# Kernel tuning notes

Measured on AMD Instinct MI355X. Metric: run time of the kernel, lower is better.

Reference implementation:

```python
import jax, jax.numpy as jnp
import numpy as np
import math

B, T, DIN, ENC_LEN, ENC, DEC = 16384, 13, 4, 48, 60, 30

def setup_inputs() -> dict:
    key = jax.random.key(0)
    ks = jax.random.split(key, 20)
    def n(k, shape, s=0.2):
        return jax.random.normal(k, shape, dtype=jnp.float32) * s
    z = lambda *s: jnp.zeros(s, dtype=jnp.float32)
    return {
        "batch_ids": jax.random.randint(ks[0], (B,), 0, 1000),
        "y": n(ks[1], (B, T, DIN), 1.0),
        "encoder_outputs": n(ks[2], (ENC_LEN, B, ENC), 1.0),
        "hidden": n(ks[3], (B, DEC), 1.0),
        "Wq": n(ks[4], (DEC, DEC)), "bq": z(DEC),
        "Wk": n(ks[5], (DEC, ENC)), "bk": z(DEC),
        "Wv": n(ks[6], (DEC, ENC)), "bv": z(DEC),
        "Wsa1": n(ks[7], (DEC // 4, 1)), "bsa1": z(DEC // 4),
        "Wsa2": n(ks[8], (DEC, DEC // 4)), "bsa2": z(DEC),
        "Wg": n(ks[9], (DEC, 2 * DEC)), "bg": z(DEC),
        "Wf1": n(ks[10], (DEC, DEC + 1)), "bf1": z(DEC),
        "Wf2": n(ks[11], (DEC // 2, DEC)), "bf2": z(DEC // 2),
        "Wf3": n(ks[12], (1, DEC // 2)), "bf3": z(1),
        "W_ih": n(ks[13], (4 * DEC, DIN + DEC)), "b_ih": z(4 * DEC),
        "W_hh": n(ks[14], (4 * DEC, DEC)), "b_hh": z(4 * DEC),
    }

def reference(batch_ids, y, encoder_outputs, hidden, Wq, bq, Wk, bk, Wv, bv,
              Wsa1, bsa1, Wsa2, bsa2, Wg, bg, Wf1, bf1, Wf2, bf2, Wf3, bf3,
              W_ih, b_ih, W_hh, b_hh):
    y_ = jnp.transpose(y, (1, 0, 2))                       # [T,B,DIN]
    enc = jnp.transpose(encoder_outputs, (1, 0, 2))        # [B,L,ENC]
    enc_spatial = enc.mean(axis=1)                          # [B,ENC] (num_turbines=1 after unsqueeze)
    # K,V are step-independent -> hoist out of the recurrence (same math as original)
    K = enc_spatial @ Wk.T + bk                             # [B,DEC]
    V = enc_spatial @ Wv.T + bv                             # [B,DEC]
    scale = 1.0 / math.sqrt(DEC)
    rnn_in0 = jnp.nan_to_num(y_[0])                         # [B,DIN], replicates NaN->0
    cell0 = jnp.zeros_like(hidden)

    def step(carry, i):
        h, c, rin = carry                                   # [B,DEC],[B,DEC],[B,DIN]
        sr = (i.astype(jnp.float32) / 12.0).reshape(1, 1)   # step ratio
        sf = jax.nn.relu(sr @ Wsa1.T + bsa1) @ Wsa2.T + bsa2  # [1,DEC] step feature
        Q = (h + sf) @ Wq.T + bq                            # [B,DEC]
        scores = jnp.sum(K * Q, axis=-1, keepdims=True) * scale  # [B,1]
        attn = jax.nn.softmax(scores, axis=-1)              # trivially ones (single turbine)
        context = attn * V                                  # [B,DEC]
        gate = jax.nn.sigmoid(jnp.concatenate([h, context], 1) @ Wg.T + bg)
        enh = gate * h + (1.0 - gate) * context
        x = jnp.concatenate([rin, enh], 1)                  # [B,DIN+DEC]
        g = x @ W_ih.T + b_ih + h @ W_hh.T + b_hh           # [B,4*DEC]
        ig, fg, gg, og = jnp.split(g, 4, axis=1)            # torch LSTM gate order i,f,g,o
        c_new = jax.nn.sigmoid(fg) * c + jax.nn.sigmoid(ig) * jnp.tanh(gg)
        h_new = jax.nn.sigmoid(og) * jnp.tanh(c_new)
        se = jnp.broadcast_to(sr, (h_new.shape[0], 1))      # [B,1] step encoding
        zfc = jax.nn.relu(jnp.concatenate([h_new, se], 1) @ Wf1.T + bf1)
        zfc = jax.nn.relu(zfc @ Wf2.T + bf2)
        out = zfc @ Wf3.T + bf3                             # [B,1]
        nxt = jax.lax.dynamic_index_in_dim(y_, i % T, axis=0, keepdims=False)  # [B,DIN]
        rin_next = jnp.concatenate([nxt[:, 1:], out], 1)    # [B,DIN]
        return (h_new, c_new, rin_next), out

    _, outs = jax.lax.scan(step, (hidden, cell0, rnn_in0), jnp.arange(1, 13))
    return outs[:, :, 0]                                    # [12,B] = cat(dim=1).transpose(0,1)
```

## Files before the change

kernel.cpp:

```cpp
#include <hip/hip_runtime.h>
#include <math.h>

#define NB 16384
typedef _Float16 f16;
typedef _Float16 f16x8 __attribute__((ext_vector_type(8)));
typedef _Float16 f16x4 __attribute__((ext_vector_type(4)));
typedef float f32x4 __attribute__((ext_vector_type(4)));

__device__ __forceinline__ float fast_sig(float v)  { return __builtin_amdgcn_rcpf(1.0f + __expf(-v)); }
__device__ __forceinline__ float fast_tanh(float v) { return 1.0f - 2.0f * __builtin_amdgcn_rcpf(1.0f + __expf(2.0f * v)); }

#define MFMA16(A, B, C) __builtin_amdgcn_mfma_f32_16x16x32_f16(A, B, C, 0, 0, 0)
#define WBAR() __builtin_amdgcn_wave_barrier()

__global__ __launch_bounds__(256) void es_kernel(
    const float* __restrict__ enc, float* __restrict__ es)
{
    const int u = blockIdx.x * 256 + threadIdx.x;
    const float4* e4 = (const float4*)enc;
    float ax = 0.f, ay = 0.f, az = 0.f, aw = 0.f;
    #pragma unroll 8
    for (int L = 0; L < 48; ++L) {
        const float4 v = e4[(size_t)L * (NB * 15) + u];
        ax += v.x; ay += v.y; az += v.z; aw += v.w;
    }
    const float s = 1.f / 48.f;
    float4 r; r.x = ax * s; r.y = ay * s; r.z = az * s; r.w = aw * s;
    ((float4*)es)[u] = r;
}

__global__ __launch_bounds__(128, 2) void decoder_kernel(
    const float* __restrict__ y,
    const float* __restrict__ enc,
    const float* __restrict__ esrc,
    const float* __restrict__ hidden,
    const float* __restrict__ Wv,  const float* __restrict__ bv,
    const float* __restrict__ Wg,  const float* __restrict__ bg,
    const float* __restrict__ Wf1, const float* __restrict__ bf1,
    const float* __restrict__ Wf2, const float* __restrict__ bf2,
    const float* __restrict__ Wf3, const float* __restrict__ bf3,
    const float* __restrict__ Wih, const float* __restrict__ bih,
    const float* __restrict__ Whh, const float* __restrict__ bhh,
    float* __restrict__ out)
{
    __shared__ __align__(16) f16 x16[16][72];
    __shared__ __align__(16) f16 z1b[16][32];

    const int t = threadIdx.x;
    const int wid = t >> 6, l = t & 63;
    const int r = l & 15, g = l >> 4;
    const int bw = blockIdx.x * 16;
    const f32x4 kz = {0.f, 0.f, 0.f, 0.f};

    #pragma unroll
    for (int d = 0; d < 5; ++d) { const int u = d * 128 + t; if (u < 576) ((unsigned*)x16)[u] = 0u; }
    #pragma unroll
    for (int d = 0; d < 2; ++d) ((unsigned*)z1b)[d * 128 + t] = 0u;

    if (esrc) {
        const float4* s4 = (const float4*)esrc + (size_t)bw * 15;
        #pragma unroll
        for (int s = 0; s < 2; ++s) {
            const int u = s * 128 + t;
            if (u < 240) {
                const float4 v = s4[u];
                const int row = u / 15, q4 = u - row * 15;
                f16x4 h = {(f16)v.x, (f16)v.y, (f16)v.z, (f16)v.w};
                *(f16x4*)&x16[row][q4 * 4] = h;
            }
        }
    } else {
        const float4* e4 = (const float4*)enc + (size_t)bw * 15;
        const float sc = 1.f / 48.f;
        #pragma unroll 1
        for (int s = 0; s < 2; ++s) {
            const int u = s * 128 + t;
            if (u < 240) {
                const int row = u / 15, q4 = u - row * 15;
                float ax = 0.f, ay = 0.f, az = 0.f, aw = 0.f;
                for (int L = 0; L < 48; ++L) {
                    const float4 v = e4[(size_t)L * (NB * 15) + u];
                    ax += v.x; ay += v.y; az += v.z; aw += v.w;
                }
                f16x4 h = {(f16)(ax*sc), (f16)(ay*sc), (f16)(az*sc), (f16)(aw*sc)};
                *(f16x4*)&x16[row][q4 * 4] = h;
            }
        }
    }

    f16x8 lf[2][8], gf[2][2], vf[2][2], f1f[2], f2f, f3f;
    float bl[8], bgv[2], bv0 = 0.f, bv1 = 0.f, bf1v[2], wf1se[2], bf2v = 0.f, bf3v = 0.f;
    float hD[2][4], VD[2][4], c[2][4] = {};
    float r0v[4] = {0.f, 0.f, 0.f, 0.f};

    if (wid == 0) {
        #pragma unroll
        for (int kt = 0; kt < 2; ++kt)
            #pragma unroll
            for (int tq = 0; tq < 8; ++tq) {
                const int gate = tq >> 1, j = (tq & 1) * 16 + r;
                const int trow = gate * 30 + j;
                f16x8 w;
                #pragma unroll
                for (int e = 0; e < 8; ++e) {
                    const int k = kt * 32 + g * 8 + e;
                    float val = 0.f;
                    if (j < 30) val = (k < 34) ? Wih[trow * 34 + k] : Whh[trow * 30 + (k - 34)];
                    w[e] = (f16)val;
                }
                lf[kt][tq] = w;
            }
        #pragma unroll
        for (int nt = 0; nt < 2; ++nt) {
            const int j = nt * 16 + r;
            f16x8 w0, w1;
            #pragma unroll
            for (int e = 0; e < 8; ++e) {
                const int kl = g * 8 + e;
                w0[e] = (f16)((j < 30 && kl >= 2) ? Wg[j * 60 + (kl - 2)] : 0.f);
                w1[e] = (f16)((j < 30 && kl < 30) ? Wg[j * 60 + 30 + kl] : 0.f);
            }
            gf[0][nt] = w0; gf[1][nt] = w1;
        }
        #pragma unroll
        for (int kt = 0; kt < 2; ++kt)
            #pragma unroll
            for (int nt = 0; nt < 2; ++nt) {
                const int j = nt * 16 + r;
                f16x8 w;
                #pragma unroll
                for (int e = 0; e < 8; ++e) {
                    const int kl = kt * 32 + g * 8 + e;
                    w[e] = (f16)((j < 30 && kl < 60) ? Wv[j * 60 + kl] : 0.f);
                }
                vf[kt][nt] = w;
            }
        #pragma unroll
        for (int tq = 0; tq < 8; ++tq) {
            const int gate = tq >> 1, j = (tq & 1) * 16 + r;
            bl[tq] = (j < 30) ? bih[gate * 30 + j] + bhh[gate * 30 + j] : 0.f;
        }
        #pragma unroll
        for (int nt = 0; nt < 2; ++nt) {
            const int j = nt * 16 + r;
            bgv[nt] = (j < 30) ? bg[j] : 0.f;
        }
        bv0 = bv[r];
        bv1 = (16 + r < 30) ? bv[16 + r] : 0.f;
        #pragma unroll
        for (int nt = 0; nt < 2; ++nt)
            #pragma unroll
            for (int q = 0; q < 4; ++q) {
                const int row = 4 * g + q, j = nt * 16 + r;
                hD[nt][q] = (j < 30) ? hidden[(size_t)(bw + row) * 30 + j] : 0.f;
            }
    } else {
        #pragma unroll
        for (int nt = 0; nt < 2; ++nt) {
            const int j = nt * 16 + r;
            f16x8 w;
            #pragma unroll
            for (int e = 0; e < 8; ++e) {
                const int kl = g * 8 + e;
                w[e] = (f16)((j < 30 && kl >= 2) ? Wf1[j * 31 + (kl - 2)] : 0.f);
            }
            f1f[nt] = w;
            bf1v[nt]  = (j < 30) ? bf1[j] : 0.f;
            wf1se[nt] = (j < 30) ? Wf1[j * 31 + 30] : 0.f;
        }
        #pragma unroll
        for (int e = 0; e < 8; ++e) {
            const int kl = g * 8 + e;
            f2f[e] = (f16)((r < 15 && kl < 30) ? Wf2[r * 30 + kl] : 0.f);
            f3f[e] = (f16)((r == 0 && kl < 15) ? Wf3[kl] : 0.f);
        }
        bf2v = (r < 15) ? bf2[r] : 0.f;
        bf3v = bf3[0];
        if (l < 16) {
            const float* yp = y + (size_t)(bw + l) * 52;
            #pragma unroll
            for (int d = 0; d < 4; ++d) {
                float v = yp[d];
                r0v[d] = (v == v) ? v : 0.f;
            }
        }
    }
    __syncthreads();

    f16x8 va;
    if (wid == 0) {
        const f16x8 ea0 = *(const f16x8*)((const char*)x16 + (size_t)r * 144 + g * 16);
        const f16x8 ea1 = *(const f16x8*)((const char*)x16 + (size_t)r * 144 + 64 + g * 16);
        f32x4 vd0 = MFMA16(ea0, vf[0][0], kz); vd0 = MFMA16(ea1, vf[1][0], vd0);
        f32x4 vd1 = MFMA16(ea0, vf[0][1], kz); vd1 = MFMA16(ea1, vf[1][1], vd1);
        #pragma unroll
        for (int q = 0; q < 4; ++q) { VD[0][q] = vd0[q] + bv0; VD[1][q] = vd1[q] + bv1; }
        #pragma unroll
        for (int nt = 0; nt < 2; ++nt)
            #pragma unroll
            for (int q = 0; q < 4; ++q)
                z1b[4 * g + q][nt * 16 + r] = (f16)VD[nt][q];
        WBAR();
        va = *(const f16x8*)((const char*)z1b + (size_t)r * 64 + g * 16);
    }
    __syncthreads();

    if (wid == 0) {
        #pragma unroll
        for (int nt = 0; nt < 2; ++nt)
            #pragma unroll
            for (int q = 0; q < 4; ++q)
                x16[4 * g + q][34 + nt * 16 + r] = (f16)hD[nt][q];
    } else {
        if (l < 16) {
            #pragma unroll
            for (int d = 0; d < 4; ++d)
                x16[l][d] = (f16)r0v[d];
        }
    }

    float py1 = 0.f, py2 = 0.f, py3 = 0.f;
    #pragma unroll 1
    for (int i = 1; i <= 12; ++i) {
        if (wid == 0) {
            const f16x8 xhg = *(const f16x8*)((const char*)x16 + (size_t)r * 144 + 64 + g * 16);
            f32x4 gd0 = MFMA16(xhg, gf[0][0], kz); gd0 = MFMA16(va, gf[1][0], gd0);
            f32x4 gd1 = MFMA16(xhg, gf[0][1], kz); gd1 = MFMA16(va, gf[1][1], gd1);
            #pragma unroll
            for (int nt = 0; nt < 2; ++nt)
                #pragma unroll
                for (int q = 0; q < 4; ++q) {
                    const float a  = (nt ? gd1[q] : gd0[q]) + bgv[nt];
                    const float gt = fast_sig(a);
                    const float enh = gt * hD[nt][q] + (1.f - gt) * VD[nt][q];
                    const int j = nt * 16 + r;
                    if (j < 30) x16[4 * g + q][4 + j] = (f16)enh;
                }
        } else if (i > 1) {
            const int s = i - 1;
            const float se = (float)s * (1.f / 12.f);
            {
                const f16x8 hn = *(const f16x8*)((const char*)x16 + (size_t)r * 144 + 64 + g * 16);
                f32x4 d0 = MFMA16(hn, f1f[0], kz);
                f32x4 d1 = MFMA16(hn, f1f[1], kz);
                #pragma unroll
                for (int nt = 0; nt < 2; ++nt)
                    #pragma unroll
                    for (int q = 0; q < 4; ++q) {
                        const float z = fmaxf((nt ? d1[q] : d0[q]) + bf1v[nt] + se * wf1se[nt], 0.f);
                        z1b[4 * g + q][nt * 16 + r] = (f16)z;
                    }
            }
            WBAR();
            {
                const f16x8 z1a = *(const f16x8*)((const char*)z1b + (size_t)r * 64 + g * 16);
                f32x4 d = MFMA16(z1a, f2f, kz);
                #pragma unroll
                for (int q = 0; q < 4; ++q)
                    z1b[4 * g + q][r] = (f16)fmaxf(d[q] + bf2v, 0.f);
            }
            WBAR();
            {
                const f16x8 z2a = *(const f16x8*)((const char*)z1b + (size_t)r * 64 + g * 16);
                f32x4 od = MFMA16(z2a, f3f, kz);
                if (r == 0) {
                    #pragma unroll
                    for (int q = 0; q < 4; ++q) {
                        const float o = od[q] + bf3v;
                        out[(size_t)(s - 1) * NB + bw + 4 * g + q] = o;
                        x16[4 * g + q][3] = (f16)o;
                    }
                }
            }
            if (l < 16) {
                x16[l][0] = (f16)py1;
                x16[l][1] = (f16)py2;
                x16[l][2] = (f16)py3;
            }
        }
        __syncthreads();

        if (wid == 0) {
            const f16x8 xa0 = *(const f16x8*)((const char*)x16 + (size_t)r * 144 + g * 16);
            const f16x8 xa1 = *(const f16x8*)((const char*)x16 + (size_t)r * 144 + 64 + g * 16);
            f32x4 ld[8];
            #pragma unroll
            for (int tq = 0; tq < 8; ++tq) {
                ld[tq] = MFMA16(xa0, lf[0][tq], kz);
                ld[tq] = MFMA16(xa1, lf[1][tq], ld[tq]);
            }
            #pragma unroll
            for (int jh = 0; jh < 2; ++jh)
                #pragma unroll
                for (int q = 0; q < 4; ++q) {
                    const float ii = fast_sig (ld[0 + jh][q] + bl[0 + jh]);
                    const float ff = fast_sig (ld[2 + jh][q] + bl[2 + jh]);
                    const float gg = fast_tanh(ld[4 + jh][q] + bl[4 + jh]);
                    const float oo = fast_sig (ld[6 + jh][q] + bl[6 + jh]);
                    const float cn = ff * c[jh][q] + ii * gg;
                    c[jh][q] = cn;
                    const float hn = oo * fast_tanh(cn);
                    hD[jh][q] = hn;
                    x16[4 * g + q][34 + jh * 16 + r] = (f16)hn;
                }
        } else {
            if (l < 16) {
                const float* yp = y + (size_t)(bw + l) * 52 + (size_t)i * 4;
                py1 = yp[1]; py2 = yp[2]; py3 = yp[3];
            }
        }
        __syncthreads();
    }

    if (wid == 1) {
        const float se = 1.0f;
        {
            const f16x8 hn = *(const f16x8*)((const char*)x16 + (size_t)r * 144 + 64 + g * 16);
            f32x4 d0 = MFMA16(hn, f1f[0], kz);
            f32x4 d1 = MFMA16(hn, f1f[1], kz);
            #pragma unroll
            for (int nt = 0; nt < 2; ++nt)
                #pragma unroll
                for (int q = 0; q < 4; ++q) {
                    const float z = fmaxf((nt ? d1[q] : d0[q]) + bf1v[nt] + se * wf1se[nt], 0.f);
                    z1b[4 * g + q][nt * 16 + r] = (f16)z;
                }
        }
        WBAR();
        {
            const f16x8 z1a = *(const f16x8*)((const char*)z1b + (size_t)r * 64 + g * 16);
            f32x4 d = MFMA16(z1a, f2f, kz);
            #pragma unroll
            for (int q = 0; q < 4; ++q)
                z1b[4 * g + q][r] = (f16)fmaxf(d[q] + bf2v, 0.f);
        }
        WBAR();
        {
            const f16x8 z2a = *(const f16x8*)((const char*)z1b + (size_t)r * 64 + g * 16);
            f32x4 od = MFMA16(z2a, f3f, kz);
            if (r == 0) {
                #pragma unroll
                for (int q = 0; q < 4; ++q)
                    out[(size_t)11 * NB + bw + 4 * g + q] = od[q] + bf3v;
            }
        }
    }
}

extern "C" void kernel_launch(void* const* d_in, const int* in_sizes, int n_in,
                              void* d_out, int out_size, void* d_ws, size_t ws_size,
                              hipStream_t stream) {
    (void)in_sizes; (void)n_in; (void)out_size;
    const float* enc = (const float*)d_in[2];
    const size_t es_bytes = (size_t)NB * 60 * sizeof(float);
    float* es = (ws_size >= es_bytes) ? (float*)d_ws : nullptr;

    if (es) {
        es_kernel<<<dim3(NB * 15 / 256), dim3(256), 0, stream>>>(enc, es);
    }
    decoder_kernel<<<dim3(NB / 16), dim3(128), 0, stream>>>(
        (const float*)d_in[1],  enc, es, (const float*)d_in[3],
        (const float*)d_in[8],  (const float*)d_in[9],
        (const float*)d_in[14], (const float*)d_in[15],
        (const float*)d_in[16], (const float*)d_in[17],
        (const float*)d_in[18], (const float*)d_in[19],
        (const float*)d_in[20], (const float*)d_in[21],
        (const float*)d_in[22], (const float*)d_in[23],
        (const float*)d_in[24], (const float*)d_in[25],
        (float*)d_out);
}
```

Measured before the change: 67.33 us.

## Halve batch rows per block to double grid size and raise occupancy

Each block now handles 8 batch rows instead of 16, so the grid doubles to 2048 blocks while each 16-row MFMA tile stays half padded. Launch bounds move to 3 blocks per SIMD, the Wv fragments are built only for the one-time V projection instead of living in registers, and the LSTM gate MFMAs are computed per half so fewer accumulators are live. The aim is more resident waves to hide the latency of the serial 12-step recurrence. The cost is that half of every MFMA and every LDS tile is wasted on padding rows, and per-block weight loading is repeated across twice as many blocks.

```diff
diff --git a/kernel.cpp b/kernel.cpp
--- a/kernel.cpp
+++ b/kernel.cpp
@@ -29,7 +29,7 @@
     ((float4*)es)[u] = r;
 }
 
-__global__ __launch_bounds__(128, 2) void decoder_kernel(
+__global__ __launch_bounds__(128, 3) void decoder_kernel(
     const float* __restrict__ y,
     const float* __restrict__ enc,
     const float* __restrict__ esrc,
@@ -49,7 +49,7 @@
     const int t = threadIdx.x;
     const int wid = t >> 6, l = t & 63;
     const int r = l & 15, g = l >> 4;
-    const int bw = blockIdx.x * 16;
+    const int bw = blockIdx.x * 8;
     const f32x4 kz = {0.f, 0.f, 0.f, 0.f};
 
     #pragma unroll
@@ -58,38 +58,29 @@
     for (int d = 0; d < 2; ++d) ((unsigned*)z1b)[d * 128 + t] = 0u;
 
     if (esrc) {
-        const float4* s4 = (const float4*)esrc + (size_t)bw * 15;
-        #pragma unroll
-        for (int s = 0; s < 2; ++s) {
-            const int u = s * 128 + t;
-            if (u < 240) {
-                const float4 v = s4[u];
-                const int row = u / 15, q4 = u - row * 15;
-                f16x4 h = {(f16)v.x, (f16)v.y, (f16)v.z, (f16)v.w};
-                *(f16x4*)&x16[row][q4 * 4] = h;
-            }
+        if (t < 120) {
+            const float4 v = ((const float4*)esrc + (size_t)bw * 15)[t];
+            const int row = t / 15, q4 = t - row * 15;
+            f16x4 h = {(f16)v.x, (f16)v.y, (f16)v.z, (f16)v.w};
+            *(f16x4*)&x16[row][q4 * 4] = h;
         }
     } else {
-        const float4* e4 = (const float4*)enc + (size_t)bw * 15;
-        const float sc = 1.f / 48.f;
-        #pragma unroll 1
-        for (int s = 0; s < 2; ++s) {
-            const int u = s * 128 + t;
-            if (u < 240) {
-                const int row = u / 15, q4 = u - row * 15;
-                float ax = 0.f, ay = 0.f, az = 0.f, aw = 0.f;
-                for (int L = 0; L < 48; ++L) {
-                    const float4 v = e4[(size_t)L * (NB * 15) + u];
-                    ax += v.x; ay += v.y; az += v.z; aw += v.w;
-                }
-                f16x4 h = {(f16)(ax*sc), (f16)(ay*sc), (f16)(az*sc), (f16)(aw*sc)};
-                *(f16x4*)&x16[row][q4 * 4] = h;
-            }
-        }
-    }
-
-    f16x8 lf[2][8], gf[2][2], vf[2][2], f1f[2], f2f, f3f;
-    float bl[8], bgv[2], bv0 = 0.f, bv1 = 0.f, bf1v[2], wf1se[2], bf2v = 0.f, bf3v = 0.f;
+        if (t < 120) {
+            const float4* e4 = (const float4*)enc + (size_t)bw * 15;
+            const float sc = 1.f / 48.f;
+            float ax = 0.f, ay = 0.f, az = 0.f, aw = 0.f;
+            for (int L = 0; L < 48; ++L) {
+                const float4 v = e4[(size_t)L * (NB * 15) + t];
+                ax += v.x; ay += v.y; az += v.z; aw += v.w;
+            }
+            const int row = t / 15, q4 = t - row * 15;
+            f16x4 h = {(f16)(ax*sc), (f16)(ay*sc), (f16)(az*sc), (f16)(aw*sc)};
+            *(f16x4*)&x16[row][q4 * 4] = h;
+        }
+    }
+
+    f16x8 lf[2][8], gf[2][2], f1f[2], f2f, f3f;
+    float bl[8], bgv[2], bf1v[2], wf1se[2], bf2v = 0.f, bf3v = 0.f;
     float hD[2][4], VD[2][4], c[2][4] = {};
     float r0v[4] = {0.f, 0.f, 0.f, 0.f};
 
@@ -123,19 +114,6 @@
             gf[0][nt] = w0; gf[1][nt] = w1;
         }
         #pragma unroll
-        for (int kt = 0; kt < 2; ++kt)
-            #pragma unroll
-            for (int nt = 0; nt < 2; ++nt) {
-                const int j = nt * 16 + r;
-                f16x8 w;
-                #pragma unroll
-                for (int e = 0; e < 8; ++e) {
-                    const int kl = kt * 32 + g * 8 + e;
-                    w[e] = (f16)((j < 30 && kl < 60) ? Wv[j * 60 + kl] : 0.f);
-                }
-                vf[kt][nt] = w;
-            }
-        #pragma unroll
         for (int tq = 0; tq < 8; ++tq) {
             const int gate = tq >> 1, j = (tq & 1) * 16 + r;
             bl[tq] = (j < 30) ? bih[gate * 30 + j] + bhh[gate * 30 + j] : 0.f;
@@ -145,14 +123,12 @@
             const int j = nt * 16 + r;
             bgv[nt] = (j < 30) ? bg[j] : 0.f;
         }
-        bv0 = bv[r];
-        bv1 = (16 + r < 30) ? bv[16 + r] : 0.f;
         #pragma unroll
         for (int nt = 0; nt < 2; ++nt)
             #pragma unroll
             for (int q = 0; q < 4; ++q) {
                 const int row = 4 * g + q, j = nt * 16 + r;
-                hD[nt][q] = (j < 30) ? hidden[(size_t)(bw + row) * 30 + j] : 0.f;
+                hD[nt][q] = (row < 8 && j < 30) ? hidden[(size_t)(bw + row) * 30 + j] : 0.f;
             }
     } else {
         #pragma unroll
@@ -176,7 +152,7 @@
         }
         bf2v = (r < 15) ? bf2[r] : 0.f;
         bf3v = bf3[0];
-        if (l < 16) {
+        if (l < 8) {
             const float* yp = y + (size_t)(bw + l) * 52;
             #pragma unroll
             for (int d = 0; d < 4; ++d) {
@@ -189,10 +165,24 @@
 
     f16x8 va;
     if (wid == 0) {
-        const f16x8 ea0 = *(const f16x8*)((const char*)x16 + (size_t)r * 144 + g * 16);
-        const f16x8 ea1 = *(const f16x8*)((const char*)x16 + (size_t)r * 144 + 64 + g * 16);
-        f32x4 vd0 = MFMA16(ea0, vf[0][0], kz); vd0 = MFMA16(ea1, vf[1][0], vd0);
-        f32x4 vd1 = MFMA16(ea0, vf[0][1], kz); vd1 = MFMA16(ea1, vf[1][1], vd1);
+        float bv0 = bv[r];
+        float bv1 = (16 + r < 30) ? bv[16 + r] : 0.f;
+        f32x4 vd0 = kz, vd1 = kz;
+        #pragma unroll
+        for (int kt = 0; kt < 2; ++kt) {
+            const f16x8 ea = *(const f16x8*)((const char*)x16 + (size_t)r * 144 + kt * 64 + g * 16);
+            #pragma unroll
+            for (int nt = 0; nt < 2; ++nt) {
+                const int j = nt * 16 + r;
+                f16x8 w;
+                #pragma unroll
+                for (int e = 0; e < 8; ++e) {
+                    const int kl = kt * 32 + g * 8 + e;
+                    w[e] = (f16)((j < 30 && kl < 60) ? Wv[j * 60 + kl] : 0.f);
+                }
+                if (nt == 0) vd0 = MFMA16(ea, w, vd0); else vd1 = MFMA16(ea, w, vd1);
+            }
+        }
         #pragma unroll
         for (int q = 0; q < 4; ++q) { VD[0][q] = vd0[q] + bv0; VD[1][q] = vd1[q] + bv1; }
         #pragma unroll
@@ -212,7 +202,7 @@
             for (int q = 0; q < 4; ++q)
                 x16[4 * g + q][34 + nt * 16 + r] = (f16)hD[nt][q];
     } else {
-        if (l < 16) {
+        if (l < 8) {
             #pragma unroll
             for (int d = 0; d < 4; ++d)
                 x16[l][d] = (f16)r0v[d];
@@ -263,7 +253,7 @@
             {
                 const f16x8 z2a = *(const f16x8*)((const char*)z1b + (size_t)r * 64 + g * 16);
                 f32x4 od = MFMA16(z2a, f3f, kz);
-                if (r == 0) {
+                if (r == 0 && g < 2) {
                     #pragma unroll
                     for (int q = 0; q < 4; ++q) {
                         const float o = od[q] + bf3v;
@@ -272,7 +262,7 @@
                     }
                 }
             }
-            if (l < 16) {
+            if (l < 8) {
                 x16[l][0] = (f16)py1;
                 x16[l][1] = (f16)py2;
                 x16[l][2] = (f16)py3;
@@ -283,28 +273,27 @@
         if (wid == 0) {
             const f16x8 xa0 = *(const f16x8*)((const char*)x16 + (size_t)r * 144 + g * 16);
             const f16x8 xa1 = *(const f16x8*)((const char*)x16 + (size_t)r * 144 + 64 + g * 16);
-            f32x4 ld[8];
-            #pragma unroll
-            for (int tq = 0; tq < 8; ++tq) {
-                ld[tq] = MFMA16(xa0, lf[0][tq], kz);
-                ld[tq] = MFMA16(xa1, lf[1][tq], ld[tq]);
-            }
-            #pragma unroll
-            for (int jh = 0; jh < 2; ++jh)
+            #pragma unroll
+            for (int jh = 0; jh < 2; ++jh) {
+                f32x4 li = MFMA16(xa0, lf[0][0 + jh], kz); li = MFMA16(xa1, lf[1][0 + jh], li);
+                f32x4 lff = MFMA16(xa0, lf[0][2 + jh], kz); lff = MFMA16(xa1, lf[1][2 + jh], lff);
+                f32x4 lg = MFMA16(xa0, lf[0][4 + jh], kz); lg = MFMA16(xa1, lf[1][4 + jh], lg);
+                f32x4 lo = MFMA16(xa0, lf[0][6 + jh], kz); lo = MFMA16(xa1, lf[1][6 + jh], lo);
                 #pragma unroll
                 for (int q = 0; q < 4; ++q) {
-                    const float ii = fast_sig (ld[0 + jh][q] + bl[0 + jh]);
-                    const float ff = fast_sig (ld[2 + jh][q] + bl[2 + jh]);
-                    const float gg = fast_tanh(ld[4 + jh][q] + bl[4 + jh]);
-                    const float oo = fast_sig (ld[6 + jh][q] + bl[6 + jh]);
+                    const float ii = fast_sig (li[q]  + bl[0 + jh]);
+                    const float ff = fast_sig (lff[q] + bl[2 + jh]);
+                    const float gg = fast_tanh(lg[q]  + bl[4 + jh]);
+                    const float oo = fast_sig (lo[q]  + bl[6 + jh]);
                     const float cn = ff * c[jh][q] + ii * gg;
                     c[jh][q] = cn;
                     const float hn = oo * fast_tanh(cn);
                     hD[jh][q] = hn;
                     x16[4 * g + q][34 + jh * 16 + r] = (f16)hn;
                 }
+            }
         } else {
-            if (l < 16) {
+            if (l < 8) {
                 const float* yp = y + (size_t)(bw + l) * 52 + (size_t)i * 4;
                 py1 = yp[1]; py2 = yp[2]; py3 = yp[3];
             }
@@ -338,7 +327,7 @@
         {
             const f16x8 z2a = *(const f16x8*)((const char*)z1b + (size_t)r * 64 + g * 16);
             f32x4 od = MFMA16(z2a, f3f, kz);
-            if (r == 0) {
+            if (r == 0 && g < 2) {
                 #pragma unroll
                 for (int q = 0; q < 4; ++q)
                     out[(size_t)11 * NB + bw + 4 * g + q] = od[q] + bf3v;
@@ -358,7 +347,7 @@
     if (es) {
         es_kernel<<<dim3(NB * 15 / 256), dim3(256), 0, stream>>>(enc, es);
     }
-    decoder_kernel<<<dim3(NB / 16), dim3(128), 0, stream>>>(
+    decoder_kernel<<<dim3(NB / 8), dim3(128), 0, stream>>>(
         (const float*)d_in[1],  enc, es, (const float*)d_in[3],
         (const float*)d_in[8],  (const float*)d_in[9],
         (const float*)d_in[14], (const float*)d_in[15],
```

Measured after the change: 116.6 us. 73.1% more time.

## Split LSTM gate MFMAs across both waves by hidden-unit half

Applied to the files above, without the earlier changes.

The LSTM gate computation, previously done entirely by wave 0 (16 MFMAs plus all activations), is split so each of the two waves computes the four gates for one 16-column half of the hidden state. Each wave keeps only its own cell-state slice, and wave 0 reads the upper half of the previous h back from shared memory for the gate blend. The Wv weight fragments are now built inline at their single use instead of being held in registers for the whole kernel, which lowers register pressure. The price is an extra barrier per step between the shared-memory reads and the writes of the new h.

```diff
diff --git a/kernel.cpp b/kernel.cpp
--- a/kernel.cpp
+++ b/kernel.cpp
@@ -88,17 +88,20 @@
         }
     }
 
-    f16x8 lf[2][8], gf[2][2], vf[2][2], f1f[2], f2f, f3f;
-    float bl[8], bgv[2], bv0 = 0.f, bv1 = 0.f, bf1v[2], wf1se[2], bf2v = 0.f, bf3v = 0.f;
-    float hD[2][4], VD[2][4], c[2][4] = {};
+    f16x8 lfW[2][4];
+    f16x8 gf[2][2], f1f[2], f2f, f3f;
+    float blW[4];
+    float bgv[2], bf1v[2], wf1se[2], bf2v = 0.f, bf3v = 0.f;
+    float hD[2][4], VD[2][4];
+    float cW[4] = {0.f, 0.f, 0.f, 0.f};
     float r0v[4] = {0.f, 0.f, 0.f, 0.f};
 
-    if (wid == 0) {
+    {
+        const int j = wid * 16 + r;
         #pragma unroll
         for (int kt = 0; kt < 2; ++kt)
             #pragma unroll
-            for (int tq = 0; tq < 8; ++tq) {
-                const int gate = tq >> 1, j = (tq & 1) * 16 + r;
+            for (int gate = 0; gate < 4; ++gate) {
                 const int trow = gate * 30 + j;
                 f16x8 w;
                 #pragma unroll
@@ -108,8 +111,14 @@
                     if (j < 30) val = (k < 34) ? Wih[trow * 34 + k] : Whh[trow * 30 + (k - 34)];
                     w[e] = (f16)val;
                 }
-                lf[kt][tq] = w;
-            }
+                lfW[kt][gate] = w;
+            }
+        #pragma unroll
+        for (int gate = 0; gate < 4; ++gate)
+            blW[gate] = (j < 30) ? bih[gate * 30 + j] + bhh[gate * 30 + j] : 0.f;
+    }
+
+    if (wid == 0) {
         #pragma unroll
         for (int nt = 0; nt < 2; ++nt) {
             const int j = nt * 16 + r;
@@ -123,30 +132,10 @@
             gf[0][nt] = w0; gf[1][nt] = w1;
         }
         #pragma unroll
-        for (int kt = 0; kt < 2; ++kt)
-            #pragma unroll
-            for (int nt = 0; nt < 2; ++nt) {
-                const int j = nt * 16 + r;
-                f16x8 w;
-                #pragma unroll
-                for (int e = 0; e < 8; ++e) {
-                    const int kl = kt * 32 + g * 8 + e;
-                    w[e] = (f16)((j < 30 && kl < 60) ? Wv[j * 60 + kl] : 0.f);
-                }
-                vf[kt][nt] = w;
-            }
-        #pragma unroll
-        for (int tq = 0; tq < 8; ++tq) {
-            const int gate = tq >> 1, j = (tq & 1) * 16 + r;
-            bl[tq] = (j < 30) ? bih[gate * 30 + j] + bhh[gate * 30 + j] : 0.f;
-        }
-        #pragma unroll
         for (int nt = 0; nt < 2; ++nt) {
             const int j = nt * 16 + r;
             bgv[nt] = (j < 30) ? bg[j] : 0.f;
         }
-        bv0 = bv[r];
-        bv1 = (16 + r < 30) ? bv[16 + r] : 0.f;
         #pragma unroll
         for (int nt = 0; nt < 2; ++nt)
             #pragma unroll
@@ -189,10 +178,24 @@
 
     f16x8 va;
     if (wid == 0) {
-        const f16x8 ea0 = *(const f16x8*)((const char*)x16 + (size_t)r * 144 + g * 16);
-        const f16x8 ea1 = *(const f16x8*)((const char*)x16 + (size_t)r * 144 + 64 + g * 16);
-        f32x4 vd0 = MFMA16(ea0, vf[0][0], kz); vd0 = MFMA16(ea1, vf[1][0], vd0);
-        f32x4 vd1 = MFMA16(ea0, vf[0][1], kz); vd1 = MFMA16(ea1, vf[1][1], vd1);
+        float bv0 = bv[r];
+        float bv1 = (16 + r < 30) ? bv[16 + r] : 0.f;
+        f32x4 vd0 = kz, vd1 = kz;
+        #pragma unroll
+        for (int kt = 0; kt < 2; ++kt) {
+            const f16x8 ea = *(const f16x8*)((const char*)x16 + (size_t)r * 144 + kt * 64 + g * 16);
+            #pragma unroll
+            for (int nt = 0; nt < 2; ++nt) {
+                const int j = nt * 16 + r;
+                f16x8 w;
+                #pragma unroll
+                for (int e = 0; e < 8; ++e) {
+                    const int kl = kt * 32 + g * 8 + e;
+                    w[e] = (f16)((j < 30 && kl < 60) ? Wv[j * 60 + kl] : 0.f);
+                }
+                if (nt == 0) vd0 = MFMA16(ea, w, vd0); else vd1 = MFMA16(ea, w, vd1);
+            }
+        }
         #pragma unroll
         for (int q = 0; q < 4; ++q) { VD[0][q] = vd0[q] + bv0; VD[1][q] = vd1[q] + bv1; }
         #pragma unroll
@@ -232,7 +235,8 @@
                 for (int q = 0; q < 4; ++q) {
                     const float a  = (nt ? gd1[q] : gd0[q]) + bgv[nt];
                     const float gt = fast_sig(a);
-                    const float enh = gt * hD[nt][q] + (1.f - gt) * VD[nt][q];
+                    const float hp = (nt == 0) ? hD[0][q] : (float)x16[4 * g + q][50 + r];
+                    const float enh = gt * hp + (1.f - gt) * VD[nt][q];
                     const int j = nt * 16 + r;
                     if (j < 30) x16[4 * g + q][4 + j] = (f16)enh;
                 }
@@ -280,34 +284,31 @@
         }
         __syncthreads();
 
-        if (wid == 0) {
-            const f16x8 xa0 = *(const f16x8*)((const char*)x16 + (size_t)r * 144 + g * 16);
-            const f16x8 xa1 = *(const f16x8*)((const char*)x16 + (size_t)r * 144 + 64 + g * 16);
-            f32x4 ld[8];
-            #pragma unroll
-            for (int tq = 0; tq < 8; ++tq) {
-                ld[tq] = MFMA16(xa0, lf[0][tq], kz);
-                ld[tq] = MFMA16(xa1, lf[1][tq], ld[tq]);
-            }
-            #pragma unroll
-            for (int jh = 0; jh < 2; ++jh)
-                #pragma unroll
-                for (int q = 0; q < 4; ++q) {
-                    const float ii = fast_sig (ld[0 + jh][q] + bl[0 + jh]);
-                    const float ff = fast_sig (ld[2 + jh][q] + bl[2 + jh]);
-                    const float gg = fast_tanh(ld[4 + jh][q] + bl[4 + jh]);
-                    const float oo = fast_sig (ld[6 + jh][q] + bl[6 + jh]);
-                    const float cn = ff * c[jh][q] + ii * gg;
-                    c[jh][q] = cn;
-                    const float hn = oo * fast_tanh(cn);
-                    hD[jh][q] = hn;
-                    x16[4 * g + q][34 + jh * 16 + r] = (f16)hn;
-                }
-        } else {
-            if (l < 16) {
-                const float* yp = y + (size_t)(bw + l) * 52 + (size_t)i * 4;
-                py1 = yp[1]; py2 = yp[2]; py3 = yp[3];
-            }
+        const f16x8 xa0 = *(const f16x8*)((const char*)x16 + (size_t)r * 144 + g * 16);
+        const f16x8 xa1 = *(const f16x8*)((const char*)x16 + (size_t)r * 144 + 64 + g * 16);
+        __syncthreads();
+
+        {
+            f32x4 li  = MFMA16(xa0, lfW[0][0], kz); li  = MFMA16(xa1, lfW[1][0], li);
+            f32x4 lff = MFMA16(xa0, lfW[0][1], kz); lff = MFMA16(xa1, lfW[1][1], lff);
+            f32x4 lg  = MFMA16(xa0, lfW[0][2], kz); lg  = MFMA16(xa1, lfW[1][2], lg);
+            f32x4 lo  = MFMA16(xa0, lfW[0][3], kz); lo  = MFMA16(xa1, lfW[1][3], lo);
+            #pragma unroll
+            for (int q = 0; q < 4; ++q) {
+                const float ii = fast_sig (li[q]  + blW[0]);
+                const float ff = fast_sig (lff[q] + blW[1]);
+                const float gg = fast_tanh(lg[q]  + blW[2]);
+                const float oo = fast_sig (lo[q]  + blW[3]);
+                const float cn = ff * cW[q] + ii * gg;
+                cW[q] = cn;
+                const float hn = oo * fast_tanh(cn);
+                if (wid == 0) hD[0][q] = hn;
+                x16[4 * g + q][34 + wid * 16 + r] = (f16)hn;
+            }
+        }
+        if (wid == 1 && l < 16) {
+            const float* yp = y + (size_t)(bw + l) * 52 + (size_t)i * 4;
+            py1 = yp[1]; py2 = yp[2]; py3 = yp[3];
         }
         __syncthreads();
     }
```

Result: slower. 69.97 us (+3.9%).
